# Kernel tuning notes

Measured on AMD Instinct MI355X. Metric: run time of the kernel, lower is better.

Reference implementation:

```python
import jax, jax.numpy as jnp
import numpy as np


def _layernorm(x, g, b, eps=1e-5):
    mu = x.mean(-1, keepdims=True)
    var = ((x - mu) ** 2).mean(-1, keepdims=True)
    return (x - mu) / jnp.sqrt(var + eps) * g + b


def _bilinear_sample(feat, coords):
    # feat: (B,C,H,W,D); coords: (B,C,N,2) normalized to [-1,1]
    # torch.grid_sample(mode='bilinear', padding_mode='zeros', align_corners=True)
    B, C, H, W, D = feat.shape
    x = (coords[..., 0] + 1.0) * 0.5 * (W - 1)  # grid x -> width axis
    y = (coords[..., 1] + 1.0) * 0.5 * (H - 1)  # grid y -> height axis
    x0 = jnp.floor(x)
    y0 = jnp.floor(y)
    wx1 = x - x0
    wy1 = y - y0
    bi = jnp.arange(B)[:, None, None]
    ci = jnp.arange(C)[None, :, None]

    def corner(yi, xi, w):
        inb = (xi >= 0) & (xi < W) & (yi >= 0) & (yi < H)
        xc = jnp.clip(xi, 0, W - 1).astype(jnp.int32)
        yc = jnp.clip(yi, 0, H - 1).astype(jnp.int32)
        v = feat[bi, ci, yc, xc]  # (B,C,N,D) gather
        return v * (w * inb)[..., None]

    return (corner(y0, x0, (1 - wy1) * (1 - wx1))
            + corner(y0, x0 + 1, (1 - wy1) * wx1)
            + corner(y0 + 1, x0, wy1 * (1 - wx1))
            + corner(y0 + 1, x0 + 1, wy1 * wx1))


def setup_inputs() -> dict:
    key = jax.random.key(0)
    ks = jax.random.split(key, 12)
    B, C, N, D, H, W = 2, 8, 16384, 256, 64, 64
    s = 1.0 / np.sqrt(D).astype(np.float32)
    return {
        "queries": jax.random.normal(ks[0], (B, N, D), jnp.float32),
        "image_features": jax.random.normal(ks[1], (B, C, H, W, D), jnp.float32),
        "pixel_coords": jax.random.uniform(ks[2], (B, C, N, 2), jnp.float32) * 2.0 - 1.0,
        "valid_mask": jax.random.randint(ks[3], (B, C, N), 0, 2).astype(jnp.int32),
        "Wq": jax.random.normal(ks[4], (D, D), jnp.float32) * s,
        "bq": jnp.zeros((D,), jnp.float32),
        "Wkv": jax.random.normal(ks[5], (D, 2 * D), jnp.float32) * s,
        "bkv": jnp.zeros((2 * D,), jnp.float32),
        "Wo": jax.random.normal(ks[6], (D, D), jnp.float32) * s,
        "bo": jnp.zeros((D,), jnp.float32),
        "gamma": jnp.ones((D,), jnp.float32),
        "beta": jnp.zeros((D,), jnp.float32),
    }


def reference(queries, image_features, pixel_coords, valid_mask,
              Wq, bq, Wkv, bkv, Wo, bo, gamma, beta):
    B, N, D = queries.shape
    residual = queries
    qn = _layernorm(queries, gamma, beta)
    sampled = _bilinear_sample(image_features, pixel_coords)      # (B,C,N,D)
    sampled = jnp.transpose(sampled, (0, 2, 1, 3))                 # (B,N,C,D)
    q = qn @ Wq + bq                                               # (B,N,D)
    kv = sampled @ Wkv + bkv                                       # (B,N,C,2D)
    k, v = kv[..., :D], kv[..., D:]
    scores = jnp.einsum('bnd,bncd->bnc', q, k) / jnp.sqrt(jnp.float32(D))
    valid = jnp.transpose(valid_mask, (0, 2, 1)) != 0              # (B,N,C)
    scores = jnp.where(valid, scores, -jnp.inf)
    attn = jax.nn.softmax(scores, axis=-1)
    attn = jnp.where(jnp.isnan(attn), 0.0, attn)                   # all-invalid -> 0
    out = jnp.einsum('bnc,bncd->bnd', attn, v)
    return residual + out @ Wo + bo
```

## Files before the change

kernel.cpp:

```cpp
#include <hip/hip_runtime.h>
#include <math.h>

#define NROWS 32768

typedef __attribute__((ext_vector_type(8))) short short8;
typedef __attribute__((ext_vector_type(4))) float f32x4;

#define WS_ABF    0
#define WS_WVOBF  32768
#define WS_PB     65536
#define WS_BVO    65792
#define WS_FEATBF 8487424

__device__ __forceinline__ unsigned short f2bf(float f) {
    unsigned u = __builtin_bit_cast(unsigned, f);
    u += 0x7FFFu + ((u >> 16) & 1u);
    return (unsigned short)(u >> 16);
}
__device__ __forceinline__ float bf_lo(unsigned u) {
    return __builtin_bit_cast(float, u << 16);
}
__device__ __forceinline__ float bf_hi(unsigned u) {
    return __builtin_bit_cast(float, u & 0xFFFF0000u);
}

__global__ __launch_bounds__(256)
void precompute_kernel(const float* __restrict__ Wq, const float* __restrict__ bq,
                       const float* __restrict__ Wkv, const float* __restrict__ bkv,
                       const float* __restrict__ Wo, const float* __restrict__ feat,
                       float* __restrict__ ws) {
    int t = threadIdx.x;
    int blk = blockIdx.x;
    if (blk >= 514) {
        long i = (long)(blk - 514) * 1024 + t * 4;
        float4 v = *(const float4*)(feat + i);
        unsigned lo = (unsigned)f2bf(v.x) | ((unsigned)f2bf(v.y) << 16);
        unsigned hi = (unsigned)f2bf(v.z) | ((unsigned)f2bf(v.w) << 16);
        *(uint2*)((unsigned short*)(ws + WS_FEATBF) + i) = make_uint2(lo, hi);
        return;
    }
    if (blk < 256) {
        int f = blk;
        const float4* wq4 = (const float4*)(Wq + f * 256);
        const float4* wk4 = (const float4*)(Wkv + (long)t * 512);
        float acc = 0.f;
        #pragma unroll 8
        for (int d4 = 0; d4 < 64; ++d4) {
            float4 a = wq4[d4], b = wk4[d4];
            acc += a.x * b.x + a.y * b.y + a.z * b.z + a.w * b.w;
        }
        ((unsigned short*)(ws + WS_ABF))[t * 256 + f] = f2bf(acc);
    } else if (blk < 512) {
        int e = blk - 256;
        float acc = 0.f;
        #pragma unroll 8
        for (int g = 0; g < 256; ++g)
            acc = fmaf(Wkv[(long)e * 512 + 256 + g], Wo[g * 256 + t], acc);
        ((unsigned short*)(ws + WS_WVOBF))[t * 256 + e] = f2bf(acc);
    } else if (blk == 512) {
        float acc = 0.f;
        #pragma unroll 8
        for (int d = 0; d < 256; ++d)
            acc = fmaf(bq[d], Wkv[(long)t * 512 + d], acc);
        ws[WS_PB + t] = acc;
    } else {
        float acc = 0.f;
        #pragma unroll 8
        for (int g = 0; g < 256; ++g)
            acc = fmaf(bkv[256 + g], Wo[g * 256 + t], acc);
        ws[WS_BVO + t] = acc;
    }
}

#define RPB  16
#define SLOT 260

__global__ __launch_bounds__(256, 4)
void fused_rowpipe(const float* __restrict__ queries, const float* __restrict__ gamma,
                   const float* __restrict__ beta, const float* __restrict__ coords,
                   const int* __restrict__ vmask, const float* __restrict__ bo,
                   const float* __restrict__ ws, float* __restrict__ out) {
    __shared__ float buf[RPB * SLOT + RPB];
    float* ssu = buf + RPB * SLOT;

    const unsigned short* Abf    = (const unsigned short*)(ws + WS_ABF);
    const unsigned short* Wvobf  = (const unsigned short*)(ws + WS_WVOBF);
    const float*          pb     = ws + WS_PB;
    const float*          bvo    = ws + WS_BVO;
    const unsigned short* featbf = (const unsigned short*)(ws + WS_FEATBF);

    int tid = threadIdx.x, wave = tid >> 6, lane = tid & 63;
    long row0 = (long)blockIdx.x * RPB;

    float4 qstash[4];

    {
        float4 g4 = *(const float4*)(gamma + 4 * lane);
        float4 b4 = *(const float4*)(beta + 4 * lane);
        #pragma unroll
        for (int rr = 0; rr < 4; ++rr) {
            int r = wave * 4 + rr;
            float4 v = *(const float4*)(queries + (row0 + r) * 256 + 4 * lane);
            qstash[rr] = v;
            float s = v.x + v.y + v.z + v.w;
            s += __shfl_xor(s, 32); s += __shfl_xor(s, 16); s += __shfl_xor(s, 8);
            s += __shfl_xor(s, 4);  s += __shfl_xor(s, 2);  s += __shfl_xor(s, 1);
            float mu = s * 0.00390625f;
            float dx = v.x - mu, dy = v.y - mu, dz = v.z - mu, dw = v.w - mu;
            float vv = dx * dx + dy * dy + dz * dz + dw * dw;
            vv += __shfl_xor(vv, 32); vv += __shfl_xor(vv, 16); vv += __shfl_xor(vv, 8);
            vv += __shfl_xor(vv, 4);  vv += __shfl_xor(vv, 2);  vv += __shfl_xor(vv, 1);
            float rstd = rsqrtf(vv * 0.00390625f + 1e-5f);
            float qx = dx * rstd * g4.x + b4.x;
            float qy = dy * rstd * g4.y + b4.y;
            float qz = dz * rstd * g4.z + b4.z;
            float qw = dw * rstd * g4.w + b4.w;
            unsigned lo = (unsigned)f2bf(qx) | ((unsigned)f2bf(qy) << 16);
            unsigned hi = (unsigned)f2bf(qz) | ((unsigned)f2bf(qw) << 16);
            *(uint2*)((unsigned short*)&buf[r * SLOT] + 4 * lane) = make_uint2(lo, hi);
        }
    }
    __syncthreads();

    int r16 = lane & 15, g = lane >> 4;
    f32x4 zero = {0.f, 0.f, 0.f, 0.f};

    {
        f32x4 acc[4];
        #pragma unroll
        for (int nt = 0; nt < 4; ++nt) acc[nt] = zero;

        #pragma unroll
        for (int ks = 0; ks < 8; ++ks) {
            short8 bfr[4], afr;
            #pragma unroll
            for (int nt = 0; nt < 4; ++nt)
                bfr[nt] = *(const short8*)(Abf + ((wave * 64 + nt * 16 + r16) << 8) + ks * 32 + g * 8);
            afr = *(const short8*)((const unsigned short*)buf + r16 * (SLOT * 2) + ks * 32 + g * 8);
            #pragma unroll
            for (int nt = 0; nt < 4; ++nt)
                acc[nt] = __builtin_amdgcn_mfma_f32_16x16x32_bf16(afr, bfr[nt], acc[nt], 0, 0, 0);
        }
        __syncthreads();

        float pbv[4];
        #pragma unroll
        for (int nt = 0; nt < 4; ++nt) pbv[nt] = pb[wave * 64 + nt * 16 + r16];
        #pragma unroll
        for (int nt = 0; nt < 4; ++nt)
            #pragma unroll
            for (int rg = 0; rg < 4; ++rg)
                buf[(g * 4 + rg) * SLOT + wave * 64 + nt * 16 + r16] = acc[nt][rg] + pbv[nt];
    }
    __syncthreads();

    for (int rr = 0; rr < 4; ++rr) {
        int r = wave * 4 + rr;
        int rowu = __builtin_amdgcn_readfirstlane((int)(row0 + r));
        int b = rowu >> 14;
        int n = rowu & 16383;

        float4 p4 = *(const float4*)(&buf[r * SLOT + 4 * lane]);

        float m = -INFINITY, ssum = 0.f;
        float4 sbacc = {0.f, 0.f, 0.f, 0.f};

        #pragma unroll
        for (int c = 0; c < 8; ++c) {
            long cb = (long)(b * 8 + c) * 16384 + n;
            float cx = coords[2 * cb];
            float cy = coords[2 * cb + 1];
            bool vld = (vmask[cb] != 0);
            float x = (cx + 1.f) * 31.5f;
            float y = (cy + 1.f) * 31.5f;
            float x0f = floorf(x), y0f = floorf(y);
            float wx = x - x0f, wy = y - y0f;
            int ix0 = (int)x0f, iy0 = (int)y0f;
            int ix1 = ix0 + 1, iy1 = iy0 + 1;
            float bx0 = (ix0 >= 0 && ix0 < 64) ? 1.f : 0.f;
            float bx1 = (ix1 >= 0 && ix1 < 64) ? 1.f : 0.f;
            float by0 = (iy0 >= 0 && iy0 < 64) ? 1.f : 0.f;
            float by1 = (iy1 >= 0 && iy1 < 64) ? 1.f : 0.f;
            int cx0 = min(max(ix0, 0), 63), cx1 = min(max(ix1, 0), 63);
            int cy0 = min(max(iy0, 0), 63), cy1 = min(max(iy1, 0), 63);
            const unsigned short* fb = featbf + ((long)(b * 8 + c) << 20);
            const uint2* r00 = (const uint2*)(fb + ((cy0 * 64 + cx0) << 8)) + lane;
            const uint2* r01 = (const uint2*)(fb + ((cy0 * 64 + cx1) << 8)) + lane;
            const uint2* r10 = (const uint2*)(fb + ((cy1 * 64 + cx0) << 8)) + lane;
            const uint2* r11 = (const uint2*)(fb + ((cy1 * 64 + cx1) << 8)) + lane;
            float w00 = (1.f - wy) * (1.f - wx) * by0 * bx0;
            float w01 = (1.f - wy) * wx * by0 * bx1;
            float w10 = wy * (1.f - wx) * by1 * bx0;
            float w11 = wy * wx * by1 * bx1;
            uint2 v00 = *r00, v01 = *r01, v10 = *r10, v11 = *r11;
            float4 s;
            s.x = w00 * bf_lo(v00.x) + w01 * bf_lo(v01.x) + w10 * bf_lo(v10.x) + w11 * bf_lo(v11.x);
            s.y = w00 * bf_hi(v00.x) + w01 * bf_hi(v01.x) + w10 * bf_hi(v10.x) + w11 * bf_hi(v11.x);
            s.z = w00 * bf_lo(v00.y) + w01 * bf_lo(v01.y) + w10 * bf_lo(v10.y) + w11 * bf_lo(v11.y);
            s.w = w00 * bf_hi(v00.y) + w01 * bf_hi(v01.y) + w10 * bf_hi(v10.y) + w11 * bf_hi(v11.y);
            float t = s.x * p4.x + s.y * p4.y + s.z * p4.z + s.w * p4.w;
            t += __shfl_xor(t, 32); t += __shfl_xor(t, 16); t += __shfl_xor(t, 8);
            t += __shfl_xor(t, 4);  t += __shfl_xor(t, 2);  t += __shfl_xor(t, 1);
            t *= 0.0625f;
            if (vld) {
                float nm = fmaxf(m, t);
                float scale = __expf(m - nm);
                float w = __expf(t - nm);
                ssum = ssum * scale + w;
                sbacc.x = fmaf(w, s.x, sbacc.x * scale);
                sbacc.y = fmaf(w, s.y, sbacc.y * scale);
                sbacc.z = fmaf(w, s.z, sbacc.z * scale);
                sbacc.w = fmaf(w, s.w, sbacc.w * scale);
                m = nm;
            }
        }

        float4 sb = {0.f, 0.f, 0.f, 0.f};
        float sa = 0.f;
        if (m > -INFINITY) {
            float inv = 1.f / ssum;
            sb.x = sbacc.x * inv;
            sb.y = sbacc.y * inv;
            sb.z = sbacc.z * inv;
            sb.w = sbacc.w * inv;
            sa = 1.f;
        }
        unsigned lo = (unsigned)f2bf(sb.x) | ((unsigned)f2bf(sb.y) << 16);
        unsigned hi = (unsigned)f2bf(sb.z) | ((unsigned)f2bf(sb.w) << 16);
        *(uint2*)((unsigned short*)&buf[r * SLOT] + 4 * lane) = make_uint2(lo, hi);
        if (lane == 0) ssu[r] = sa;
    }
    __syncthreads();

    {
        f32x4 acc2[4];
        #pragma unroll
        for (int nt = 0; nt < 4; ++nt) acc2[nt] = zero;

        #pragma unroll
        for (int ks = 0; ks < 8; ++ks) {
            short8 bfr[4], afr;
            #pragma unroll
            for (int nt = 0; nt < 4; ++nt)
                bfr[nt] = *(const short8*)(Wvobf + ((wave * 64 + nt * 16 + r16) << 8) + ks * 32 + g * 8);
            afr = *(const short8*)((const unsigned short*)buf + r16 * (SLOT * 2) + ks * 32 + g * 8);
            #pragma unroll
            for (int nt = 0; nt < 4; ++nt)
                acc2[nt] = __builtin_amdgcn_mfma_f32_16x16x32_bf16(afr, bfr[nt], acc2[nt], 0, 0, 0);
        }
        __syncthreads();

        #pragma unroll
        for (int nt = 0; nt < 4; ++nt)
            #pragma unroll
            for (int rg = 0; rg < 4; ++rg)
                buf[(g * 4 + rg) * SLOT + wave * 64 + nt * 16 + r16] = acc2[nt][rg];
    }
    __syncthreads();

    {
        float4 bvo4 = *(const float4*)(bvo + 4 * lane);
        float4 bo4  = *(const float4*)(bo + 4 * lane);
        #pragma unroll
        for (int rr = 0; rr < 4; ++rr) {
            int r = wave * 4 + rr;
            float4 q4 = qstash[rr];
            float4 a4 = *(const float4*)(&buf[r * SLOT + 4 * lane]);
            float su = ssu[r];
            float4 o;
            o.x = q4.x + a4.x + su * bvo4.x + bo4.x;
            o.y = q4.y + a4.y + su * bvo4.y + bo4.y;
            o.z = q4.z + a4.z + su * bvo4.z + bo4.z;
            o.w = q4.w + a4.w + su * bvo4.w + bo4.w;
            *(float4*)(out + (row0 + r) * 256 + 4 * lane) = o;
        }
    }
}

extern "C" void kernel_launch(void* const* d_in, const int* in_sizes, int n_in,
                              void* d_out, int out_size, void* d_ws, size_t ws_size,
                              hipStream_t stream) {
    const float* queries = (const float*)d_in[0];
    const float* feat    = (const float*)d_in[1];
    const float* coords  = (const float*)d_in[2];
    const int*   vmask   = (const int*)  d_in[3];
    const float* Wq      = (const float*)d_in[4];
    const float* bq      = (const float*)d_in[5];
    const float* Wkv     = (const float*)d_in[6];
    const float* bkv     = (const float*)d_in[7];
    const float* Wo      = (const float*)d_in[8];
    const float* bo      = (const float*)d_in[9];
    const float* gamma   = (const float*)d_in[10];
    const float* beta    = (const float*)d_in[11];
    float* out = (float*)d_out;
    float* ws  = (float*)d_ws;

    precompute_kernel<<<514 + 16384, 256, 0, stream>>>(Wq, bq, Wkv, bkv, Wo, feat, ws);
    fused_rowpipe<<<NROWS / RPB, 256, 0, stream>>>(queries, gamma, beta, coords, vmask, bo, ws, out);
}
```

Before: 287.7 us.

## Double rows per block to 32 with 512 threads and 2x2 MFMA tiles

The fused row kernel now handles 32 rows per block using 8 waves. Each wave computes a 2x2 tile of 16x16 MFMA outputs covering 32 rows and 32 columns, so each weight fragment loaded from global memory is reused across two row tiles, roughly halving weight traffic per row. The feature-to-bf16 conversion blocks now process 16 elements per thread with 128-bit stores, cutting the block count by four. Larger blocks need more LDS and registers per block, which may lower occupancy; the launch bounds of (512, 8) may also force register limits and cause spills.

After: 267.5 us, median of 2. -7.0%, faster.

```diff
diff --git a/kernel.cpp b/kernel.cpp
--- a/kernel.cpp
+++ b/kernel.cpp
@@ -32,11 +32,19 @@
     int t = threadIdx.x;
     int blk = blockIdx.x;
     if (blk >= 514) {
-        long i = (long)(blk - 514) * 1024 + t * 4;
-        float4 v = *(const float4*)(feat + i);
-        unsigned lo = (unsigned)f2bf(v.x) | ((unsigned)f2bf(v.y) << 16);
-        unsigned hi = (unsigned)f2bf(v.z) | ((unsigned)f2bf(v.w) << 16);
-        *(uint2*)((unsigned short*)(ws + WS_FEATBF) + i) = make_uint2(lo, hi);
+        long i = (long)(blk - 514) * 4096 + t * 16;
+        const float4* src = (const float4*)(feat + i);
+        unsigned short* dst = (unsigned short*)(ws + WS_FEATBF) + i;
+        #pragma unroll
+        for (int h = 0; h < 2; ++h) {
+            float4 a = src[2 * h], b = src[2 * h + 1];
+            uint4 o;
+            o.x = (unsigned)f2bf(a.x) | ((unsigned)f2bf(a.y) << 16);
+            o.y = (unsigned)f2bf(a.z) | ((unsigned)f2bf(a.w) << 16);
+            o.z = (unsigned)f2bf(b.x) | ((unsigned)f2bf(b.y) << 16);
+            o.w = (unsigned)f2bf(b.z) | ((unsigned)f2bf(b.w) << 16);
+            *(uint4*)(dst + 8 * h) = o;
+        }
         return;
     }
     if (blk < 256) {
@@ -72,10 +80,10 @@
     }
 }
 
-#define RPB  16
+#define RPB  32
 #define SLOT 260
 
-__global__ __launch_bounds__(256, 4)
+__global__ __launch_bounds__(512, 8)
 void fused_rowpipe(const float* __restrict__ queries, const float* __restrict__ gamma,
                    const float* __restrict__ beta, const float* __restrict__ coords,
                    const int* __restrict__ vmask, const float* __restrict__ bo,
@@ -126,31 +134,40 @@
     f32x4 zero = {0.f, 0.f, 0.f, 0.f};
 
     {
-        f32x4 acc[4];
-        #pragma unroll
-        for (int nt = 0; nt < 4; ++nt) acc[nt] = zero;
+        f32x4 acc[2][2];
+        #pragma unroll
+        for (int mt = 0; mt < 2; ++mt)
+            #pragma unroll
+            for (int nt = 0; nt < 2; ++nt) acc[mt][nt] = zero;
 
         #pragma unroll
         for (int ks = 0; ks < 8; ++ks) {
-            short8 bfr[4], afr;
-            #pragma unroll
-            for (int nt = 0; nt < 4; ++nt)
-                bfr[nt] = *(const short8*)(Abf + ((wave * 64 + nt * 16 + r16) << 8) + ks * 32 + g * 8);
-            afr = *(const short8*)((const unsigned short*)buf + r16 * (SLOT * 2) + ks * 32 + g * 8);
-            #pragma unroll
-            for (int nt = 0; nt < 4; ++nt)
-                acc[nt] = __builtin_amdgcn_mfma_f32_16x16x32_bf16(afr, bfr[nt], acc[nt], 0, 0, 0);
+            short8 bfr[2], afr[2];
+            #pragma unroll
+            for (int nt = 0; nt < 2; ++nt)
+                bfr[nt] = *(const short8*)(Abf + ((wave * 32 + nt * 16 + r16) << 8) + ks * 32 + g * 8);
+            #pragma unroll
+            for (int mt = 0; mt < 2; ++mt)
+                afr[mt] = *(const short8*)((const unsigned short*)buf + (mt * 16 + r16) * (SLOT * 2) + ks * 32 + g * 8);
+            #pragma unroll
+            for (int mt = 0; mt < 2; ++mt)
+                #pragma unroll
+                for (int nt = 0; nt < 2; ++nt)
+                    acc[mt][nt] = __builtin_amdgcn_mfma_f32_16x16x32_bf16(afr[mt], bfr[nt], acc[mt][nt], 0, 0, 0);
         }
         __syncthreads();
 
-        float pbv[4];
-        #pragma unroll
-        for (int nt = 0; nt < 4; ++nt) pbv[nt] = pb[wave * 64 + nt * 16 + r16];
-        #pragma unroll
-        for (int nt = 0; nt < 4; ++nt)
-            #pragma unroll
-            for (int rg = 0; rg < 4; ++rg)
-                buf[(g * 4 + rg) * SLOT + wave * 64 + nt * 16 + r16] = acc[nt][rg] + pbv[nt];
+        float pbv[2];
+        #pragma unroll
+        for (int nt = 0; nt < 2; ++nt) pbv[nt] = pb[wave * 32 + nt * 16 + r16];
+        #pragma unroll
+        for (int mt = 0; mt < 2; ++mt)
+            #pragma unroll
+            for (int nt = 0; nt < 2; ++nt)
+                #pragma unroll
+                for (int rg = 0; rg < 4; ++rg)
+                    buf[(mt * 16 + g * 4 + rg) * SLOT + wave * 32 + nt * 16 + r16] =
+                        acc[mt][nt][rg] + pbv[nt];
     }
     __syncthreads();
 
@@ -233,28 +250,36 @@
     __syncthreads();
 
     {
-        f32x4 acc2[4];
-        #pragma unroll
-        for (int nt = 0; nt < 4; ++nt) acc2[nt] = zero;
+        f32x4 acc2[2][2];
+        #pragma unroll
+        for (int mt = 0; mt < 2; ++mt)
+            #pragma unroll
+            for (int nt = 0; nt < 2; ++nt) acc2[mt][nt] = zero;
 
         #pragma unroll
         for (int ks = 0; ks < 8; ++ks) {
-            short8 bfr[4], afr;
-            #pragma unroll
-            for (int nt = 0; nt < 4; ++nt)
-                bfr[nt] = *(const short8*)(Wvobf + ((wave * 64 + nt * 16 + r16) << 8) + ks * 32 + g * 8);
-            afr = *(const short8*)((const unsigned short*)buf + r16 * (SLOT * 2) + ks * 32 + g * 8);
-            #pragma unroll
-            for (int nt = 0; nt < 4; ++nt)
-                acc2[nt] = __builtin_amdgcn_mfma_f32_16x16x32_bf16(afr, bfr[nt], acc2[nt], 0, 0, 0);
+            short8 bfr[2], afr[2];
+            #pragma unroll
+            for (int nt = 0; nt < 2; ++nt)
+                bfr[nt] = *(const short8*)(Wvobf + ((wave * 32 + nt * 16 + r16) << 8) + ks * 32 + g * 8);
+            #pragma unroll
+            for (int mt = 0; mt < 2; ++mt)
+                afr[mt] = *(const short8*)((const unsigned short*)buf + (mt * 16 + r16) * (SLOT * 2) + ks * 32 + g * 8);
+            #pragma unroll
+            for (int mt = 0; mt < 2; ++mt)
+                #pragma unroll
+                for (int nt = 0; nt < 2; ++nt)
+                    acc2[mt][nt] = __builtin_amdgcn_mfma_f32_16x16x32_bf16(afr[mt], bfr[nt], acc2[mt][nt], 0, 0, 0);
         }
         __syncthreads();
 
         #pragma unroll
-        for (int nt = 0; nt < 4; ++nt)
-            #pragma unroll
-            for (int rg = 0; rg < 4; ++rg)
-                buf[(g * 4 + rg) * SLOT + wave * 64 + nt * 16 + r16] = acc2[nt][rg];
+        for (int mt = 0; mt < 2; ++mt)
+            #pragma unroll
+            for (int nt = 0; nt < 2; ++nt)
+                #pragma unroll
+                for (int rg = 0; rg < 4; ++rg)
+                    buf[(mt * 16 + g * 4 + rg) * SLOT + wave * 32 + nt * 16 + r16] = acc2[mt][nt][rg];
     }
     __syncthreads();
 
@@ -295,6 +320,6 @@
     float* out = (float*)d_out;
     float* ws  = (float*)d_ws;
 
-    precompute_kernel<<<514 + 16384, 256, 0, stream>>>(Wq, bq, Wkv, bkv, Wo, feat, ws);
-    fused_rowpipe<<<NROWS / RPB, 256, 0, stream>>>(queries, gamma, beta, coords, vmask, bo, ws, out);
-}
+    precompute_kernel<<<514 + 4096, 256, 0, stream>>>(Wq, bq, Wkv, bkv, Wo, feat, ws);
+    fused_rowpipe<<<NROWS / RPB, 512, 0, stream>>>(queries, gamma, beta, coords, vmask, bo, ws, out);
+}
```
